# Kernel tuning notes

Hardware: AMD Instinct MI355X
Metric: run time of the kernel (lower is better)

Reference implementation:

```python
import jax, jax.numpy as jnp
import numpy as np
from jax.ops import segment_sum, segment_max

N = 524288        # total nodes
D = 256           # input_dim
H = 128           # output_dim (attention hidden)
B = 2048          # number of graphs (segments)


def setup_inputs() -> dict:
    key = jax.random.key(0)
    k1, k2, k3, k4, k5, k6 = jax.random.split(key, 6)
    x = jax.random.normal(k1, (N, D), dtype=jnp.float32)
    batch = jnp.sort(jax.random.randint(k2, (N,), 0, B, dtype=jnp.int64))
    # PyTorch Linear default init: U(-1/sqrt(fan_in), 1/sqrt(fan_in))
    s1 = 1.0 / np.sqrt(D)
    s2 = 1.0 / np.sqrt(H)
    W1 = jax.random.uniform(k3, (D, H), jnp.float32, -s1, s1)
    b1 = jax.random.uniform(k4, (H,), jnp.float32, -s1, s1)
    W2 = jax.random.uniform(k5, (H, 1), jnp.float32, -s2, s2)
    b2 = jax.random.uniform(k6, (1,), jnp.float32, -s2, s2)
    return {"x": x, "batch": batch, "W1": W1, "b1": b1, "W2": W2, "b2": b2}


def reference(x, batch, W1, b1, W2, b2):
    # attention MLP: Linear -> tanh -> Linear  => scores [N]
    scores = (jnp.tanh(x @ W1 + b1) @ W2 + b2)[:, 0]
    # per-graph (segment) softmax over nodes, numerically stable
    seg_max = segment_max(scores, batch, num_segments=B)          # [B]
    # empty segments give -inf max; they contribute no nodes anyway
    shifted = scores - seg_max[batch]
    expw = jnp.exp(shifted)
    denom = segment_sum(expw, batch, num_segments=B)              # [B]
    w = expw / denom[batch]                                       # [N]
    # weighted sum pooling -> [B, D]; empty segments naturally yield zeros
    pooled = segment_sum(x * w[:, None], batch, num_segments=B)
    return pooled
```

## Files before the change

kernel.cpp:

```cpp
#include <hip/hip_runtime.h>
#include <math.h>

#define DD 256
#define HH 128
#define NT 8

typedef short bf16x8 __attribute__((ext_vector_type(8)));
typedef float f32x4  __attribute__((ext_vector_type(4)));

__device__ __forceinline__ unsigned short f32_to_bf16_rne(float f) {
    unsigned u = __float_as_uint(f);
    unsigned r = u + 0x7FFFu + ((u >> 16) & 1u);
    return (unsigned short)(r >> 16);
}
__device__ __forceinline__ void split_bf16(float f, unsigned short& hi,
                                           unsigned short& lo) {
    unsigned u = __float_as_uint(f);
    unsigned r = u + 0x7FFFu + ((u >> 16) & 1u);
    hi = (unsigned short)(r >> 16);
    float hf = __uint_as_float(r & 0xFFFF0000u);
    lo = f32_to_bf16_rne(f - hf);
}
__device__ __forceinline__ float tanh_fast(float a) {
    float e = __expf(2.0f * a);
    return 1.0f - __fdividef(2.0f, e + 1.0f);
}

__global__ __launch_bounds__(256) void pack_w1_kernel(
    const float* __restrict__ W1, unsigned short* __restrict__ Wpk)
{
    int tid = blockIdx.x * 256 + threadIdx.x;
    int i  = tid & 7;
    int l  = (tid >> 3) & 63;
    int nt = (tid >> 9) & 7;
    int t  = tid >> 12;
    int k = t * 32 + ((l >> 4) << 3) + i;
    int j = nt * 16 + (l & 15);
    unsigned short hb, lb;
    split_bf16(W1[k * HH + j], hb, lb);
    Wpk[tid]         = hb;
    Wpk[32768 + tid] = lb;
}

__global__ __launch_bounds__(256) void scores_mfma_kernel(
    const float* __restrict__ x, const unsigned short* __restrict__ Wpk,
    const float* __restrict__ b1, const float* __restrict__ W2,
    const float* __restrict__ b2, float* __restrict__ scores, int n)
{
    __shared__ unsigned short lds[2][8192];

    const int w   = threadIdx.x >> 6;
    const int l   = threadIdx.x & 63;
    const int lhi = l >> 4;
    const int llo = l & 15;
    const int rowbase = blockIdx.x * 128 + w * 32;

    auto stage = [&](int t, int b) {
#pragma unroll
        for (int q = 0; q < 4; ++q) {
            int idx = w * 4 + q;
            int s = idx >> 3, c = idx & 7;
            const bf16x8* g = (const bf16x8*)(Wpk + (size_t)s * 32768 +
                                              t * 4096 + c * 512 + l * 8);
            *(bf16x8*)&lds[b][s * 4096 + c * 512 + l * 8] = *g;
        }
    };

    float4 xa[2], xb[2];
    auto load_x = [&](int t) {
#pragma unroll
        for (int mt = 0; mt < 2; ++mt) {
            int row = rowbase + mt * 16 + llo;
            if (row > n - 1) row = n - 1;
            const float* xp = x + (size_t)row * DD + t * 32 + lhi * 8;
            xa[mt] = *(const float4*)xp;
            xb[mt] = *(const float4*)(xp + 4);
        }
    };

    f32x4 acc[2][NT];
#pragma unroll
    for (int mt = 0; mt < 2; ++mt)
#pragma unroll
        for (int nt = 0; nt < NT; ++nt) acc[mt][nt] = (f32x4){0.f, 0.f, 0.f, 0.f};

    load_x(0);
    stage(0, 0);

    for (int t = 0; t < 8; ++t) {
        __syncthreads();
        if (t < 7) stage(t + 1, (t + 1) & 1);

        bf16x8 ah[2], al[2];
#pragma unroll
        for (int mt = 0; mt < 2; ++mt) {
            float xv[8] = {xa[mt].x, xa[mt].y, xa[mt].z, xa[mt].w,
                           xb[mt].x, xb[mt].y, xb[mt].z, xb[mt].w};
#pragma unroll
            for (int i = 0; i < 8; ++i) {
                unsigned short hb, lb;
                split_bf16(xv[i], hb, lb);
                ah[mt][i] = (short)hb;
                al[mt][i] = (short)lb;
            }
        }
        if (t < 7) load_x(t + 1);

        const int b = t & 1;
#pragma unroll
        for (int nt = 0; nt < NT; ++nt) {
            bf16x8 bh = *(const bf16x8*)&lds[b][0 * 4096 + nt * 512 + l * 8];
            bf16x8 bl = *(const bf16x8*)&lds[b][1 * 4096 + nt * 512 + l * 8];
#pragma unroll
            for (int mt = 0; mt < 2; ++mt) {
                acc[mt][nt] = __builtin_amdgcn_mfma_f32_16x16x32_bf16(ah[mt], bh, acc[mt][nt], 0, 0, 0);
                acc[mt][nt] = __builtin_amdgcn_mfma_f32_16x16x32_bf16(ah[mt], bl, acc[mt][nt], 0, 0, 0);
                acc[mt][nt] = __builtin_amdgcn_mfma_f32_16x16x32_bf16(al[mt], bh, acc[mt][nt], 0, 0, 0);
            }
        }
    }

    const float b2v = b2[0];
    float b1v[NT], w2v[NT];
#pragma unroll
    for (int nt = 0; nt < NT; ++nt) {
        b1v[nt] = b1[nt * 16 + llo];
        w2v[nt] = W2[nt * 16 + llo];
    }
#pragma unroll
    for (int mt = 0; mt < 2; ++mt) {
#pragma unroll
        for (int r = 0; r < 4; ++r) {
            float v = 0.f;
#pragma unroll
            for (int nt = 0; nt < NT; ++nt)
                v = fmaf(tanh_fast(acc[mt][nt][r] + b1v[nt]), w2v[nt], v);
            v += __shfl_xor(v, 1);
            v += __shfl_xor(v, 2);
            v += __shfl_xor(v, 4);
            v += __shfl_xor(v, 8);
            int node = rowbase + mt * 16 + lhi * 4 + r;
            if (llo == 0 && node < n) scores[node] = v + b2v;
        }
    }
}

__device__ __forceinline__ int lower_bound_i32(const int* __restrict__ arr,
                                               int n, int val)
{
    int lo = 0, hi = n;
    while (lo < hi) {
        int mid = (lo + hi) >> 1;
        if (arr[mid] < val) lo = mid + 1; else hi = mid;
    }
    return lo;
}

__global__ __launch_bounds__(256) void seg_softmax_kernel(
    float* __restrict__ scores, const int* __restrict__ batch,
    int* __restrict__ seg_start, int* __restrict__ seg_end, int n)
{
    int b = blockIdx.x;
    int start = lower_bound_i32(batch, n, b);
    int end   = lower_bound_i32(batch, n, b + 1);
    int tid = threadIdx.x;
    int wid = tid >> 6;

    __shared__ float redmax[4];
    __shared__ float redsum[4];

    float m = -INFINITY;
    for (int i = start + tid; i < end; i += 256) m = fmaxf(m, scores[i]);
#pragma unroll
    for (int o = 32; o > 0; o >>= 1) m = fmaxf(m, __shfl_xor(m, o));
    if ((tid & 63) == 0) redmax[wid] = m;
    __syncthreads();
    m = fmaxf(fmaxf(redmax[0], redmax[1]), fmaxf(redmax[2], redmax[3]));

    float sum = 0.f;
    for (int i = start + tid; i < end; i += 256) sum += expf(scores[i] - m);
#pragma unroll
    for (int o = 32; o > 0; o >>= 1) sum += __shfl_xor(sum, o);
    if ((tid & 63) == 0) redsum[wid] = sum;
    __syncthreads();
    sum = redsum[0] + redsum[1] + redsum[2] + redsum[3];

    float inv = (end > start) ? 1.0f / sum : 0.f;
    for (int i = start + tid; i < end; i += 256)
        scores[i] = expf(scores[i] - m) * inv;

    if (tid == 0) { seg_start[b] = start; seg_end[b] = end; }
}

__global__ __launch_bounds__(256) void pool_kernel(
    const float* __restrict__ x, const float* __restrict__ w,
    const int* __restrict__ seg_start, const int* __restrict__ seg_end,
    float* __restrict__ out)
{
    int b = blockIdx.x;
    int d = threadIdx.x;
    int start = seg_start[b];
    int end   = seg_end[b];

    float acc = 0.f;
    int i = start;
    for (; i + 4 <= end; i += 4) {
        float w0 = w[i], w1 = w[i + 1], w2 = w[i + 2], w3 = w[i + 3];
        acc = fmaf(x[(size_t)(i + 0) * DD + d], w0, acc);
        acc = fmaf(x[(size_t)(i + 1) * DD + d], w1, acc);
        acc = fmaf(x[(size_t)(i + 2) * DD + d], w2, acc);
        acc = fmaf(x[(size_t)(i + 3) * DD + d], w3, acc);
    }
    for (; i < end; ++i)
        acc = fmaf(x[(size_t)i * DD + d], w[i], acc);

    out[(size_t)b * DD + d] = acc;
}

extern "C" void kernel_launch(void* const* d_in, const int* in_sizes, int n_in,
                              void* d_out, int out_size, void* d_ws, size_t ws_size,
                              hipStream_t stream)
{
    const float* x     = (const float*)d_in[0];
    const int*   batch = (const int*)  d_in[1];
    const float* W1    = (const float*)d_in[2];
    const float* b1    = (const float*)d_in[3];
    const float* W2    = (const float*)d_in[4];
    const float* b2    = (const float*)d_in[5];
    float* out = (float*)d_out;

    int n    = in_sizes[1];
    int Bseg = out_size / DD;

    float* scores    = (float*)d_ws;
    int*   seg_start = (int*)((char*)d_ws + (size_t)n * 4);
    int*   seg_end   = seg_start + Bseg;
    unsigned short* Wpk = (unsigned short*)((char*)d_ws + (size_t)n * 4 + (size_t)Bseg * 8);

    pack_w1_kernel<<<128, 256, 0, stream>>>(W1, Wpk);
    scores_mfma_kernel<<<(n + 127) / 128, 256, 0, stream>>>(x, Wpk, b1, W2, b2,
                                                            scores, n);
    seg_softmax_kernel<<<Bseg, 256, 0, stream>>>(scores, batch,
                                                 seg_start, seg_end, n);
    pool_kernel<<<Bseg, 256, 0, stream>>>(x, scores, seg_start, seg_end, out);
}
```

Baseline: 834.4 us.

## Read W1 fragments directly from global, double-buffer x, widen pool unroll

The scores kernel drops LDS staging of the packed W1 and its per-step __syncthreads. Each wave now reads its bf16 W1 fragments straight from global memory, relying on cache since the data is small and shared. x tiles are double-buffered in registers with the K loop fully unrolled, so next-step loads are issued early. The pool kernel unroll grows from 4 to 8 rows so more independent x loads are in flight, at the cost of higher register pressure and repeated global or L2 reads of W1 per wave.

```diff
diff --git a/kernel.cpp b/kernel.cpp
--- a/kernel.cpp
+++ b/kernel.cpp
@@ -3,7 +3,6 @@
 
 #define DD 256
 #define HH 128
-#define NT 8
 
 typedef short bf16x8 __attribute__((ext_vector_type(8)));
 typedef float f32x4  __attribute__((ext_vector_type(4)));
@@ -47,55 +46,42 @@
     const float* __restrict__ b1, const float* __restrict__ W2,
     const float* __restrict__ b2, float* __restrict__ scores, int n)
 {
-    __shared__ unsigned short lds[2][8192];
-
     const int w   = threadIdx.x >> 6;
     const int l   = threadIdx.x & 63;
     const int lhi = l >> 4;
     const int llo = l & 15;
     const int rowbase = blockIdx.x * 128 + w * 32;
 
-    auto stage = [&](int t, int b) {
-#pragma unroll
-        for (int q = 0; q < 4; ++q) {
-            int idx = w * 4 + q;
-            int s = idx >> 3, c = idx & 7;
-            const bf16x8* g = (const bf16x8*)(Wpk + (size_t)s * 32768 +
-                                              t * 4096 + c * 512 + l * 8);
-            *(bf16x8*)&lds[b][s * 4096 + c * 512 + l * 8] = *g;
-        }
-    };
-
-    float4 xa[2], xb[2];
-    auto load_x = [&](int t) {
+    f32x4 acc[2][8];
+#pragma unroll
+    for (int mt = 0; mt < 2; ++mt)
+#pragma unroll
+        for (int nt = 0; nt < 8; ++nt) acc[mt][nt] = (f32x4){0.f, 0.f, 0.f, 0.f};
+
+    float4 xa[2][2], xb[2][2];
+    auto load_x = [&](int t, int buf) {
 #pragma unroll
         for (int mt = 0; mt < 2; ++mt) {
             int row = rowbase + mt * 16 + llo;
             if (row > n - 1) row = n - 1;
             const float* xp = x + (size_t)row * DD + t * 32 + lhi * 8;
-            xa[mt] = *(const float4*)xp;
-            xb[mt] = *(const float4*)(xp + 4);
+            xa[buf][mt] = *(const float4*)xp;
+            xb[buf][mt] = *(const float4*)(xp + 4);
         }
     };
 
-    f32x4 acc[2][NT];
-#pragma unroll
-    for (int mt = 0; mt < 2; ++mt)
-#pragma unroll
-        for (int nt = 0; nt < NT; ++nt) acc[mt][nt] = (f32x4){0.f, 0.f, 0.f, 0.f};
-
-    load_x(0);
-    stage(0, 0);
-
+    load_x(0, 0);
+
+#pragma unroll
     for (int t = 0; t < 8; ++t) {
-        __syncthreads();
-        if (t < 7) stage(t + 1, (t + 1) & 1);
+        const int cur = t & 1;
+        if (t < 7) load_x(t + 1, cur ^ 1);
 
         bf16x8 ah[2], al[2];
 #pragma unroll
         for (int mt = 0; mt < 2; ++mt) {
-            float xv[8] = {xa[mt].x, xa[mt].y, xa[mt].z, xa[mt].w,
-                           xb[mt].x, xb[mt].y, xb[mt].z, xb[mt].w};
+            float xv[8] = {xa[cur][mt].x, xa[cur][mt].y, xa[cur][mt].z, xa[cur][mt].w,
+                           xb[cur][mt].x, xb[cur][mt].y, xb[cur][mt].z, xb[cur][mt].w};
 #pragma unroll
             for (int i = 0; i < 8; ++i) {
                 unsigned short hb, lb;
@@ -104,26 +90,29 @@
                 al[mt][i] = (short)lb;
             }
         }
-        if (t < 7) load_x(t + 1);
-
-        const int b = t & 1;
-#pragma unroll
-        for (int nt = 0; nt < NT; ++nt) {
-            bf16x8 bh = *(const bf16x8*)&lds[b][0 * 4096 + nt * 512 + l * 8];
-            bf16x8 bl = *(const bf16x8*)&lds[b][1 * 4096 + nt * 512 + l * 8];
-#pragma unroll
-            for (int mt = 0; mt < 2; ++mt) {
-                acc[mt][nt] = __builtin_amdgcn_mfma_f32_16x16x32_bf16(ah[mt], bh, acc[mt][nt], 0, 0, 0);
-                acc[mt][nt] = __builtin_amdgcn_mfma_f32_16x16x32_bf16(ah[mt], bl, acc[mt][nt], 0, 0, 0);
-                acc[mt][nt] = __builtin_amdgcn_mfma_f32_16x16x32_bf16(al[mt], bh, acc[mt][nt], 0, 0, 0);
+
+        const unsigned short* wp = Wpk + t * 4096 + l * 8;
+#pragma unroll
+        for (int half = 0; half < 2; ++half) {
+#pragma unroll
+            for (int q = 0; q < 4; ++q) {
+                const int nt = half * 4 + q;
+                bf16x8 bh = *(const bf16x8*)(wp + nt * 512);
+                bf16x8 bl = *(const bf16x8*)(wp + nt * 512 + 32768);
+#pragma unroll
+                for (int mt = 0; mt < 2; ++mt) {
+                    acc[mt][nt] = __builtin_amdgcn_mfma_f32_16x16x32_bf16(ah[mt], bh, acc[mt][nt], 0, 0, 0);
+                    acc[mt][nt] = __builtin_amdgcn_mfma_f32_16x16x32_bf16(ah[mt], bl, acc[mt][nt], 0, 0, 0);
+                    acc[mt][nt] = __builtin_amdgcn_mfma_f32_16x16x32_bf16(al[mt], bh, acc[mt][nt], 0, 0, 0);
+                }
             }
         }
     }
 
     const float b2v = b2[0];
-    float b1v[NT], w2v[NT];
-#pragma unroll
-    for (int nt = 0; nt < NT; ++nt) {
+    float b1v[8], w2v[8];
+#pragma unroll
+    for (int nt = 0; nt < 8; ++nt) {
         b1v[nt] = b1[nt * 16 + llo];
         w2v[nt] = W2[nt * 16 + llo];
     }
@@ -133,7 +122,7 @@
         for (int r = 0; r < 4; ++r) {
             float v = 0.f;
 #pragma unroll
-            for (int nt = 0; nt < NT; ++nt)
+            for (int nt = 0; nt < 8; ++nt)
                 v = fmaf(tanh_fast(acc[mt][nt][r] + b1v[nt]), w2v[nt], v);
             v += __shfl_xor(v, 1);
             v += __shfl_xor(v, 2);
@@ -204,12 +193,14 @@
 
     float acc = 0.f;
     int i = start;
-    for (; i + 4 <= end; i += 4) {
-        float w0 = w[i], w1 = w[i + 1], w2 = w[i + 2], w3 = w[i + 3];
-        acc = fmaf(x[(size_t)(i + 0) * DD + d], w0, acc);
-        acc = fmaf(x[(size_t)(i + 1) * DD + d], w1, acc);
-        acc = fmaf(x[(size_t)(i + 2) * DD + d], w2, acc);
-        acc = fmaf(x[(size_t)(i + 3) * DD + d], w3, acc);
+    for (; i + 8 <= end; i += 8) {
+        float wv[8], xv[8];
+#pragma unroll
+        for (int q = 0; q < 8; ++q) wv[q] = w[i + q];
+#pragma unroll
+        for (int q = 0; q < 8; ++q) xv[q] = x[(size_t)(i + q) * DD + d];
+#pragma unroll
+        for (int q = 0; q < 8; ++q) acc = fmaf(xv[q], wv[q], acc);
     }
     for (; i < end; ++i)
         acc = fmaf(x[(size_t)i * DD + d], w[i], acc);
```

After: 902.2 us. +8.1%, slower.
